# Kernel tuning notes

Hardware: AMD Instinct MI355X
Metric: run time of the kernel (lower is better)

## Reference

```python
import jax, jax.numpy as jnp
import numpy as np

N, M, H, K, C_IN, C_OUT, P_DIM = 25000, 25000, 32, 15, 128, 128, 3
KP_EXTENT = 1.2
RADIUS = 2.5


def setup_inputs() -> dict:
    key = jax.random.key(0)
    k1, k2, k3, k4, k5, k6 = jax.random.split(key, 6)
    x = jax.random.normal(k1, (M, C_IN), dtype=jnp.float32)
    q_pts = jax.random.uniform(k2, (N, P_DIM), dtype=jnp.float32) * (2.0 * RADIUS)
    s_pts = jax.random.uniform(k3, (M, P_DIM), dtype=jnp.float32) * (2.0 * RADIUS)
    # indices in [0, M]; index == M is the shadow neighbor
    neighb_inds = jax.random.randint(k4, (N, H), 0, M + 1, dtype=jnp.int64)
    # kernel points roughly inside the sphere of given radius
    kernel_points = jax.random.normal(k5, (K, P_DIM), dtype=jnp.float32) * (RADIUS * 0.5)
    # kaiming-like scale for weights [K, C_in, C_out]
    weights = jax.random.normal(k6, (K, C_IN, C_OUT), dtype=jnp.float32) * (1.0 / np.sqrt(C_IN))
    return {"x": x, "q_pts": q_pts, "s_pts": s_pts, "neighb_inds": neighb_inds,
            "kernel_points": kernel_points, "weights": weights}


def reference(x, q_pts, s_pts, neighb_inds, kernel_points, weights):
    # Add shadow point far away and zero shadow feature row
    s_pad = jnp.concatenate([s_pts, jnp.full((1, P_DIM), 1e6, dtype=s_pts.dtype)], axis=0)
    x_pad = jnp.concatenate([x, jnp.zeros((1, C_IN), dtype=x.dtype)], axis=0)

    # neighbors relative to each query point: [N, H, p_dim]
    neighbors = s_pad[neighb_inds] - q_pts[:, None, :]
    # differences to kernel points: [N, H, K, p_dim]
    differences = neighbors[:, :, None, :] - kernel_points[None, None, :, :]
    sq_distances = jnp.sum(differences * differences, axis=-1)  # [N, H, K]

    # linear influence, clipped at 0
    all_weights = jnp.clip(1.0 - jnp.sqrt(sq_distances) / KP_EXTENT, 0.0, None)
    all_weights = jnp.transpose(all_weights, (0, 2, 1))  # [N, K, H]

    neighb_x = x_pad[neighb_inds]                        # [N, H, C_in]
    weighted_features = jnp.matmul(all_weights, neighb_x)  # [N, K, C_in]

    # per-kernel-point matmul and sum over kernel points
    out = jnp.einsum('nkc,kcd->nd', weighted_features, weights)  # [N, C_out]
    return out
```

## Files before the change

### kernel.cpp

```cpp
#include <hip/hip_runtime.h>
#include <hip/hip_bf16.h>

#define N_Q   25000
#define M_S   25000
#define C_INV 128

typedef unsigned short ushortT;
typedef unsigned short us8 __attribute__((ext_vector_type(8)));
typedef unsigned short us4 __attribute__((ext_vector_type(4)));
typedef short s8v __attribute__((ext_vector_type(8)));
typedef float f32x4 __attribute__((ext_vector_type(4)));

#define GAS __attribute__((address_space(1)))
#define LAS __attribute__((address_space(3)))

__device__ __forceinline__ float b2f(ushortT u) {
    unsigned v = ((unsigned)u) << 16;
    return __builtin_bit_cast(float, v);
}
__device__ __forceinline__ ushortT f2b(float f) {
    __hip_bfloat16 h = __float2bfloat16(f);
    return __builtin_bit_cast(ushortT, h);
}

__global__ void k_convert_x(const float* __restrict__ x, ushortT* __restrict__ xb) {
    int i = blockIdx.x * 256 + threadIdx.x;
    const int n4 = (M_S * C_INV) / 4;
    if (i >= n4) return;
    float4 v = ((const float4*)x)[i];
    us4 o;
    o[0] = f2b(v.x); o[1] = f2b(v.y); o[2] = f2b(v.z); o[3] = f2b(v.w);
    ((us4*)xb)[i] = o;
}

__global__ void k_build_wfrag2(const float* __restrict__ W, ushortT* __restrict__ wf) {
    int o = blockIdx.x * 256 + threadIdx.x;
    if (o >= 262144) return;
    int j   = o & 7;
    int l   = (o >> 3) & 63;
    int db  = (o >> 9) & 7;
    int ks  = o >> 12;
    int p   = ks * 32 + ((l >> 4) * 8) + j;
    int ci  = p >> 8;
    int rem = p & 255;
    int ls  = rem >> 2;
    int r   = rem & 3;
    int k   = (ls >> 4) * 4 + r;
    int c   = ci * 16 + (ls & 15);
    int d   = db * 16 + (l & 15);
    wf[o] = (k < 15) ? f2b(W[((size_t)k * 128 + c) * 128 + d]) : (ushortT)0;
}

__global__ void k_build_wfrag(const float* __restrict__ W, ushortT* __restrict__ wf) {
    int o = blockIdx.x * 256 + threadIdx.x;
    if (o >= 1920 * 128) return;
    int j  = o & 7;
    int l  = (o >> 3) & 63;
    int db = (o >> 9) & 7;
    int ks = o >> 12;
    int r  = ks * 32 + ((l >> 4) * 8) + j;
    int d  = db * 16 + (l & 15);
    wf[o] = f2b(W[r * 128 + d]);
}

__global__ __launch_bounds__(512, 4) void k_ab(
    const float* __restrict__ qp, const float* __restrict__ sp,
    const int* __restrict__ nb, const float* __restrict__ kp,
    const ushortT* __restrict__ xbf, ushortT* __restrict__ wf_out)
{
    __shared__ __align__(16) ushortT s_w[16 * 512];
    __shared__ int s_idx[16 * 32];

    const int t   = threadIdx.x;
    const int l   = t & 63;
    const int w   = t >> 6;
    const int blk = blockIdx.x;

    {
        const int q  = t >> 5;
        const int h  = t & 31;
        const int qg = blk * 16 + q;
        const int qc = (qg < N_Q) ? qg : (N_Q - 1);
        const float qx = qp[qc * 3 + 0], qy = qp[qc * 3 + 1], qz = qp[qc * 3 + 2];
        int idx = (qg < N_Q) ? nb[qg * 32 + h] : M_S;
        const bool valid = ((unsigned)idx < (unsigned)M_S);
        const int idc = valid ? idx : 0;
        s_idx[q * 32 + h] = idc;
        float px, py, pz;
        if (valid) { px = sp[idc * 3]; py = sp[idc * 3 + 1]; pz = sp[idc * 3 + 2]; }
        else       { px = 1e6f; py = 1e6f; pz = 1e6f; }
        const float rx = px - qx, ry = py - qy, rz = pz - qz;
        #pragma unroll
        for (int k = 0; k < 15; ++k) {
            const float dx = rx - kp[k * 3 + 0];
            const float dy = ry - kp[k * 3 + 1];
            const float dz = rz - kp[k * 3 + 2];
            const float d2 = dx * dx + dy * dy + dz * dz;
            float wv = 1.0f - sqrtf(d2) * (1.0f / 1.2f);
            wv = (wv > 0.0f) ? wv : 0.0f;
            s_w[q * 512 + (h >> 3) * 128 + k * 8 + (h & 7)] = f2b(wv);
        }
        s_w[q * 512 + (h >> 3) * 128 + 15 * 8 + (h & 7)] = 0;
    }
    __syncthreads();

    const int c0 = l & 15;
    const int hg = l >> 4;

    s8v af[2];
    int ridx[2][8];
    #pragma unroll
    for (int qi = 0; qi < 2; ++qi) {
        const int q = w * 2 + qi;
        af[qi] = *(const s8v*)(s_w + q * 512 + hg * 128 + c0 * 8);
        #pragma unroll
        for (int j = 0; j < 8; ++j)
            ridx[qi][j] = s_idx[q * 32 + hg * 8 + j];
    }

    us4* wfo = (us4*)wf_out;

    #pragma unroll
    for (int qi = 0; qi < 2; ++qi) {
        const int qrow = blk * 16 + w * 2 + qi;
        const ushortT* rp[8];
        #pragma unroll
        for (int j = 0; j < 8; ++j)
            rp[j] = xbf + (size_t)ridx[qi][j] * 128 + c0;

        us8 xr[8];
        #pragma unroll
        for (int j = 0; j < 8; ++j) {
            #pragma unroll
            for (int ci = 0; ci < 8; ++ci)
                xr[ci][j] = rp[j][ci * 16];
        }
        #pragma unroll
        for (int ci = 0; ci < 8; ++ci) {
            f32x4 d = __builtin_amdgcn_mfma_f32_16x16x32_bf16(
                af[qi], __builtin_bit_cast(s8v, xr[ci]), (f32x4){0.f, 0.f, 0.f, 0.f}, 0, 0, 0);
            us4 o;
            o[0] = f2b(d[0]); o[1] = f2b(d[1]); o[2] = f2b(d[2]); o[3] = f2b(d[3]);
            wfo[(size_t)qrow * 512 + ci * 64 + l] = o;
        }
    }
}

__global__ __launch_bounds__(512, 4) void k_gemm(
    const ushortT* __restrict__ wf, const ushortT* __restrict__ wfrag,
    float* __restrict__ out)
{
    __shared__ __align__(16) ushortT sA[2][8192];

    const int t   = threadIdx.x;
    const int l   = t & 63;
    const int w   = t >> 6;
    const int blk = blockIdx.x;
    const int qg  = w >> 2;
    const int n0  = (w & 3) * 2;

    auto stage = [&](int c4, int buf) {
        #pragma unroll
        for (int u = 0; u < 2; ++u) {
            const int s    = u * 512 + t;
            const int q    = s >> 4;
            const int part = s & 15;
            const ushortT* src = wf + (size_t)(blk * 64 + q) * 2048 + c4 * 128
                               + ((part ^ (q & 7)) * 8);
            __builtin_amdgcn_global_load_lds((const GAS unsigned int*)(const void*)src,
                                             (LAS unsigned int*)(void*)(&sA[buf][(size_t)s * 8]),
                                             16, 0, 0);
        }
    };

    f32x4 a00 = {0.f,0.f,0.f,0.f}, a01 = {0.f,0.f,0.f,0.f};
    f32x4 a10 = {0.f,0.f,0.f,0.f}, a11 = {0.f,0.f,0.f,0.f};

    stage(0, 0);
    __syncthreads();

    for (int c4 = 0; c4 < 16; ++c4) {
        if (c4 < 15) stage(c4 + 1, (c4 + 1) & 1);
        const ushortT* A = sA[c4 & 1];
        const int q0 = qg * 32 + (l & 15);
        const int q1 = q0 + 16;
        #pragma unroll
        for (int kk = 0; kk < 4; ++kk) {
            const int ks = c4 * 4 + kk;
            const s8v b0 = *(const s8v*)(wfrag + ((size_t)(ks * 8 + n0    ) * 64 + l) * 8);
            const s8v b1 = *(const s8v*)(wfrag + ((size_t)(ks * 8 + n0 + 1) * 64 + l) * 8);
            const int eo = kk * 32 + (l >> 4) * 8;
            const s8v av0 = *(const s8v*)(A + q0 * 128 + (eo ^ ((q0 & 7) * 8)));
            const s8v av1 = *(const s8v*)(A + q1 * 128 + (eo ^ ((q1 & 7) * 8)));
            a00 = __builtin_amdgcn_mfma_f32_16x16x32_bf16(av0, b0, a00, 0, 0, 0);
            a01 = __builtin_amdgcn_mfma_f32_16x16x32_bf16(av0, b1, a01, 0, 0, 0);
            a10 = __builtin_amdgcn_mfma_f32_16x16x32_bf16(av1, b0, a10, 0, 0, 0);
            a11 = __builtin_amdgcn_mfma_f32_16x16x32_bf16(av1, b1, a11, 0, 0, 0);
        }
        __syncthreads();
    }

    #pragma unroll
    for (int r = 0; r < 4; ++r) {
        const int qa = blk * 64 + qg * 32 + (l >> 4) * 4 + r;
        const int qb = qa + 16;
        const int d0 = n0 * 16 + (l & 15);
        if (qa < N_Q) {
            out[(size_t)qa * 128 + d0]      = a00[r];
            out[(size_t)qa * 128 + d0 + 16] = a01[r];
        }
        if (qb < N_Q) {
            out[(size_t)qb * 128 + d0]      = a10[r];
            out[(size_t)qb * 128 + d0 + 16] = a11[r];
        }
    }
}

__global__ __launch_bounds__(256, 2) void k_main_fb(
    const float* __restrict__ qp, const float* __restrict__ sp,
    const int* __restrict__ nb, const float* __restrict__ kp,
    const ushortT* __restrict__ xbf, const ushortT* __restrict__ wfrag,
    float* __restrict__ out)
{
    __shared__ ushortT s_w[16][32][16];
    __shared__ int s_idx[16][32];
    __shared__ __align__(16) ushortT s_wf[16][1928];

    const int t   = threadIdx.x;
    const int blk = blockIdx.x;

    {
        const int q  = t >> 4;
        const int h0 = t & 15;
        const int qg = blk * 16 + q;
        const int qc = (qg < N_Q) ? qg : 0;
        const float qx = qp[qc * 3 + 0], qy = qp[qc * 3 + 1], qz = qp[qc * 3 + 2];
        #pragma unroll
        for (int i = 0; i < 2; ++i) {
            const int h  = h0 + 16 * i;
            int idx = (qg < N_Q) ? nb[qg * 32 + h] : M_S;
            const bool valid = ((unsigned)idx < (unsigned)M_S);
            s_idx[q][h] = valid ? idx : 0;
            float px, py, pz;
            if (valid) { px = sp[idx * 3]; py = sp[idx * 3 + 1]; pz = sp[idx * 3 + 2]; }
            else       { px = 1e6f; py = 1e6f; pz = 1e6f; }
            const float rx = px - qx, ry = py - qy, rz = pz - qz;
            #pragma unroll
            for (int k = 0; k < 15; ++k) {
                const float dx = rx - kp[k * 3 + 0];
                const float dy = ry - kp[k * 3 + 1];
                const float dz = rz - kp[k * 3 + 2];
                const float d2 = dx * dx + dy * dy + dz * dz;
                float wv = 1.0f - sqrtf(d2) * (1.0f / 1.2f);
                wv = (wv > 0.0f) ? wv : 0.0f;
                s_w[q][h][k] = f2b(wv);
            }
            s_w[q][h][15] = 0;
        }
    }
    __syncthreads();

    {
        const int q  = t >> 4;
        const int c0 = (t & 15) * 8;
        float acc[15][8];
        #pragma unroll
        for (int k = 0; k < 15; ++k)
            #pragma unroll
            for (int j = 0; j < 8; ++j) acc[k][j] = 0.0f;

        int idx0 = s_idx[q][0];
        us8 xv = *(const us8*)(xbf + (size_t)idx0 * C_INV + c0);
        for (int h = 0; h < 32; ++h) {
            const us8 xc = xv;
            if (h < 31) {
                int idn = s_idx[q][h + 1];
                xv = *(const us8*)(xbf + (size_t)idn * C_INV + c0);
            }
            const us8 w0 = *(const us8*)&s_w[q][h][0];
            const us8 w1 = *(const us8*)&s_w[q][h][8];
            float xf[8];
            #pragma unroll
            for (int j = 0; j < 8; ++j) xf[j] = b2f(xc[j]);
            #pragma unroll
            for (int k = 0; k < 15; ++k) {
                const float wk = b2f((k < 8) ? w0[k] : w1[k - 8]);
                #pragma unroll
                for (int j = 0; j < 8; ++j) acc[k][j] += wk * xf[j];
            }
        }
        #pragma unroll
        for (int k = 0; k < 15; ++k) {
            us8 o;
            #pragma unroll
            for (int j = 0; j < 8; ++j) o[j] = f2b(acc[k][j]);
            *(us8*)&s_wf[q][k * C_INV + c0] = o;
        }
    }
    __syncthreads();

    {
        const int lane = t & 63;
        const int wv   = t >> 6;
        const int db0  = wv * 2;
        const int arow = lane & 15;
        const int kofs = (lane >> 4) * 8;
        f32x4 acc0 = {0.f, 0.f, 0.f, 0.f};
        f32x4 acc1 = {0.f, 0.f, 0.f, 0.f};
        #pragma unroll 4
        for (int ks = 0; ks < 60; ++ks) {
            s8v a  = *(const s8v*)&s_wf[arow][ks * 32 + kofs];
            s8v b0 = *(const s8v*)(wfrag + ((size_t)(ks * 8 + db0) * 64 + lane) * 8);
            s8v b1 = *(const s8v*)(wfrag + ((size_t)(ks * 8 + db0 + 1) * 64 + lane) * 8);
            acc0 = __builtin_amdgcn_mfma_f32_16x16x32_bf16(a, b0, acc0, 0, 0, 0);
            acc1 = __builtin_amdgcn_mfma_f32_16x16x32_bf16(a, b1, acc1, 0, 0, 0);
        }
        #pragma unroll
        for (int r = 0; r < 4; ++r) {
            const int q  = (lane >> 4) * 4 + r;
            const int qg = blk * 16 + q;
            if (qg < N_Q) {
                out[(size_t)qg * 128 + db0 * 16 + (lane & 15)]       = acc0[r];
                out[(size_t)qg * 128 + (db0 + 1) * 16 + (lane & 15)] = acc1[r];
            }
        }
    }
}

extern "C" void kernel_launch(void* const* d_in, const int* in_sizes, int n_in,
                              void* d_out, int out_size, void* d_ws, size_t ws_size,
                              hipStream_t stream) {
    const float* x  = (const float*)d_in[0];
    const float* qp = (const float*)d_in[1];
    const float* sp = (const float*)d_in[2];
    const int*   nb = (const int*)d_in[3];
    const float* kp = (const float*)d_in[4];
    const float* W  = (const float*)d_in[5];
    float* out = (float*)d_out;

    const size_t xbf_b   = (size_t)M_S * C_INV * 2;
    const size_t wfrag_b = (size_t)2048 * 128 * 2;
    const size_t wf_b    = (size_t)25024 * 2048 * 2;

    ushortT* xbf   = (ushortT*)d_ws;
    ushortT* wfrag = (ushortT*)((char*)d_ws + xbf_b);
    ushortT* wfbuf = (ushortT*)((char*)d_ws + xbf_b + wfrag_b);

    k_convert_x<<<3125, 256, 0, stream>>>(x, xbf);

    if (ws_size >= xbf_b + wfrag_b + wf_b) {
        k_build_wfrag2<<<1024, 256, 0, stream>>>(W, wfrag);
        k_ab<<<(N_Q + 15) / 16, 512, 0, stream>>>(qp, sp, nb, kp, xbf, wfbuf);
        k_gemm<<<(N_Q + 63) / 64, 512, 0, stream>>>(wfbuf, wfrag, out);
    } else {
        k_build_wfrag<<<960, 256, 0, stream>>>(W, wfrag);
        k_main_fb<<<(N_Q + 15) / 16, 256, 0, stream>>>(qp, sp, nb, kp, xbf, wfrag, out);
    }
}
```

Before: 81.14 us.

## Gather neighbor features via LDS transpose reads and split-K gemm with atomics

The gather stage now uses 256-thread blocks of 8 queries. Neighbor feature rows are loaded with coalesced global_load_lds into LDS and then read back with ds_read_b64_tr_b16 to form MFMA B operands, replacing the scattered per-element 2-byte global loads. The second gemm drops its LDS staging in favor of direct global loads and splits the K dimension four ways across blocks, accumulating into a pre-zeroed output with float atomics. This targets the uncoalesced gather and raises parallelism in the gemm, at the cost of an extra zeroing kernel, atomic traffic, and dropped bounds checks in the gather kernel.

```diff
diff --git a/kernel.cpp b/kernel.cpp
--- a/kernel.cpp
+++ b/kernel.cpp
@@ -21,6 +21,12 @@
 __device__ __forceinline__ ushortT f2b(float f) {
     __hip_bfloat16 h = __float2bfloat16(f);
     return __builtin_bit_cast(ushortT, h);
+}
+__device__ __forceinline__ s8v mk8(us4 a, us4 b) {
+    us8 r;
+    r[0] = a[0]; r[1] = a[1]; r[2] = a[2]; r[3] = a[3];
+    r[4] = b[0]; r[5] = b[1]; r[6] = b[2]; r[7] = b[3];
+    return __builtin_bit_cast(s8v, r);
 }
 
 __global__ void k_convert_x(const float* __restrict__ x, ushortT* __restrict__ xb) {
@@ -63,13 +69,20 @@
     wf[o] = f2b(W[r * 128 + d]);
 }
 
-__global__ __launch_bounds__(512, 4) void k_ab(
+__global__ void k_zero(float* __restrict__ out) {
+    int i = blockIdx.x * 256 + threadIdx.x;
+    if (i < (N_Q * 128) / 4)
+        ((float4*)out)[i] = float4{0.f, 0.f, 0.f, 0.f};
+}
+
+__global__ __launch_bounds__(256, 6) void k_ab(
     const float* __restrict__ qp, const float* __restrict__ sp,
     const int* __restrict__ nb, const float* __restrict__ kp,
     const ushortT* __restrict__ xbf, ushortT* __restrict__ wf_out)
 {
-    __shared__ __align__(16) ushortT s_w[16 * 512];
-    __shared__ int s_idx[16 * 32];
+    __shared__ __align__(16) ushortT s_w[8 * 512];
+    __shared__ int s_idx[8 * 32];
+    __shared__ __align__(16) ushortT s_x[4][2048];
 
     const int t   = threadIdx.x;
     const int l   = t & 63;
@@ -79,10 +92,9 @@
     {
         const int q  = t >> 5;
         const int h  = t & 31;
-        const int qg = blk * 16 + q;
-        const int qc = (qg < N_Q) ? qg : (N_Q - 1);
-        const float qx = qp[qc * 3 + 0], qy = qp[qc * 3 + 1], qz = qp[qc * 3 + 2];
-        int idx = (qg < N_Q) ? nb[qg * 32 + h] : M_S;
+        const int qg = blk * 8 + q;
+        const float qx = qp[qg * 3 + 0], qy = qp[qg * 3 + 1], qz = qp[qg * 3 + 2];
+        int idx = nb[qg * 32 + h];
         const bool valid = ((unsigned)idx < (unsigned)M_S);
         const int idc = valid ? idx : 0;
         s_idx[q * 32 + h] = idc;
@@ -104,114 +116,115 @@
     }
     __syncthreads();
 
-    const int c0 = l & 15;
-    const int hg = l >> 4;
-
-    s8v af[2];
-    int ridx[2][8];
-    #pragma unroll
+    const int g = l >> 4;
+    const int c = l & 15;
+    us4* wfo = (us4*)wf_out;
+
+    LAS ushortT* trp = (LAS ushortT*)(void*)(&s_x[w][g * 128 + c * 4]);
+
     for (int qi = 0; qi < 2; ++qi) {
-        const int q = w * 2 + qi;
-        af[qi] = *(const s8v*)(s_w + q * 512 + hg * 128 + c0 * 8);
-        #pragma unroll
-        for (int j = 0; j < 8; ++j)
-            ridx[qi][j] = s_idx[q * 32 + hg * 8 + j];
-    }
-
-    us4* wfo = (us4*)wf_out;
-
-    #pragma unroll
-    for (int qi = 0; qi < 2; ++qi) {
-        const int qrow = blk * 16 + w * 2 + qi;
-        const ushortT* rp[8];
-        #pragma unroll
-        for (int j = 0; j < 8; ++j)
-            rp[j] = xbf + (size_t)ridx[qi][j] * 128 + c0;
-
-        us8 xr[8];
-        #pragma unroll
-        for (int j = 0; j < 8; ++j) {
-            #pragma unroll
-            for (int ci = 0; ci < 8; ++ci)
-                xr[ci][j] = rp[j][ci * 16];
-        }
-        #pragma unroll
-        for (int ci = 0; ci < 8; ++ci) {
-            f32x4 d = __builtin_amdgcn_mfma_f32_16x16x32_bf16(
-                af[qi], __builtin_bit_cast(s8v, xr[ci]), (f32x4){0.f, 0.f, 0.f, 0.f}, 0, 0, 0);
-            us4 o;
-            o[0] = f2b(d[0]); o[1] = f2b(d[1]); o[2] = f2b(d[2]); o[3] = f2b(d[3]);
-            wfo[(size_t)qrow * 512 + ci * 64 + l] = o;
-        }
-    }
-}
-
-__global__ __launch_bounds__(512, 4) void k_gemm(
+        const int q    = w * 2 + qi;
+        const int qrow = blk * 8 + q;
+        const s8v af   = *(const s8v*)(s_w + q * 512 + g * 128 + c * 8);
+        const int myid = s_idx[q * 32 + (l >> 1)];
+        const ushortT* srcb = xbf + (size_t)myid * 128 + (l & 1) * 8;
+
+        #pragma unroll
+        for (int hf = 0; hf < 2; ++hf) {
+            #pragma unroll
+            for (int ci = 0; ci < 4; ++ci) {
+                __builtin_amdgcn_global_load_lds(
+                    (const GAS unsigned int*)(const void*)(srcb + (hf * 4 + ci) * 16),
+                    (LAS unsigned int*)(void*)(&s_x[w][ci * 512]), 16, 0, 0);
+            }
+            asm volatile("s_waitcnt vmcnt(0)" ::: "memory");
+            __builtin_amdgcn_sched_barrier(0);
+
+            us4 ta0, tb0, ta1, tb1, ta2, tb2, ta3, tb3;
+            asm volatile(
+                "ds_read_b64_tr_b16 %0, %8 offset:0\n\t"
+                "ds_read_b64_tr_b16 %1, %8 offset:128\n\t"
+                "ds_read_b64_tr_b16 %2, %8 offset:1024\n\t"
+                "ds_read_b64_tr_b16 %3, %8 offset:1152\n\t"
+                "ds_read_b64_tr_b16 %4, %8 offset:2048\n\t"
+                "ds_read_b64_tr_b16 %5, %8 offset:2176\n\t"
+                "ds_read_b64_tr_b16 %6, %8 offset:3072\n\t"
+                "ds_read_b64_tr_b16 %7, %8 offset:3200\n\t"
+                "s_waitcnt lgkmcnt(0)"
+                : "=&v"(ta0), "=&v"(tb0), "=&v"(ta1), "=&v"(tb1),
+                  "=&v"(ta2), "=&v"(tb2), "=&v"(ta3), "=&v"(tb3)
+                : "v"(trp));
+            __builtin_amdgcn_sched_barrier(0);
+
+            const s8v b0 = mk8(ta0, tb0);
+            const s8v b1 = mk8(ta1, tb1);
+            const s8v b2 = mk8(ta2, tb2);
+            const s8v b3 = mk8(ta3, tb3);
+
+            #pragma unroll
+            for (int ci = 0; ci < 4; ++ci) {
+                const s8v bf = (ci == 0) ? b0 : (ci == 1) ? b1 : (ci == 2) ? b2 : b3;
+                f32x4 d = __builtin_amdgcn_mfma_f32_16x16x32_bf16(
+                    af, bf, (f32x4){0.f, 0.f, 0.f, 0.f}, 0, 0, 0);
+                us4 o;
+                o[0] = f2b(d[0]); o[1] = f2b(d[1]); o[2] = f2b(d[2]); o[3] = f2b(d[3]);
+                wfo[(size_t)qrow * 512 + (hf * 4 + ci) * 64 + l] = o;
+            }
+        }
+    }
+}
+
+__global__ __launch_bounds__(256, 6) void k_gemm(
     const ushortT* __restrict__ wf, const ushortT* __restrict__ wfrag,
     float* __restrict__ out)
 {
-    __shared__ __align__(16) ushortT sA[2][8192];
-
-    const int t   = threadIdx.x;
-    const int l   = t & 63;
-    const int w   = t >> 6;
-    const int blk = blockIdx.x;
-    const int qg  = w >> 2;
-    const int n0  = (w & 3) * 2;
-
-    auto stage = [&](int c4, int buf) {
-        #pragma unroll
-        for (int u = 0; u < 2; ++u) {
-            const int s    = u * 512 + t;
-            const int q    = s >> 4;
-            const int part = s & 15;
-            const ushortT* src = wf + (size_t)(blk * 64 + q) * 2048 + c4 * 128
-                               + ((part ^ (q & 7)) * 8);
-            __builtin_amdgcn_global_load_lds((const GAS unsigned int*)(const void*)src,
-                                             (LAS unsigned int*)(void*)(&sA[buf][(size_t)s * 8]),
-                                             16, 0, 0);
-        }
-    };
-
-    f32x4 a00 = {0.f,0.f,0.f,0.f}, a01 = {0.f,0.f,0.f,0.f};
-    f32x4 a10 = {0.f,0.f,0.f,0.f}, a11 = {0.f,0.f,0.f,0.f};
-
-    stage(0, 0);
-    __syncthreads();
-
-    for (int c4 = 0; c4 < 16; ++c4) {
-        if (c4 < 15) stage(c4 + 1, (c4 + 1) & 1);
-        const ushortT* A = sA[c4 & 1];
-        const int q0 = qg * 32 + (l & 15);
-        const int q1 = q0 + 16;
-        #pragma unroll
-        for (int kk = 0; kk < 4; ++kk) {
-            const int ks = c4 * 4 + kk;
-            const s8v b0 = *(const s8v*)(wfrag + ((size_t)(ks * 8 + n0    ) * 64 + l) * 8);
-            const s8v b1 = *(const s8v*)(wfrag + ((size_t)(ks * 8 + n0 + 1) * 64 + l) * 8);
-            const int eo = kk * 32 + (l >> 4) * 8;
-            const s8v av0 = *(const s8v*)(A + q0 * 128 + (eo ^ ((q0 & 7) * 8)));
-            const s8v av1 = *(const s8v*)(A + q1 * 128 + (eo ^ ((q1 & 7) * 8)));
-            a00 = __builtin_amdgcn_mfma_f32_16x16x32_bf16(av0, b0, a00, 0, 0, 0);
-            a01 = __builtin_amdgcn_mfma_f32_16x16x32_bf16(av0, b1, a01, 0, 0, 0);
-            a10 = __builtin_amdgcn_mfma_f32_16x16x32_bf16(av1, b0, a10, 0, 0, 0);
-            a11 = __builtin_amdgcn_mfma_f32_16x16x32_bf16(av1, b1, a11, 0, 0, 0);
-        }
-        __syncthreads();
+    const int t    = threadIdx.x;
+    const int l    = t & 63;
+    const int w    = t >> 6;
+    const int blk  = blockIdx.x;
+    const int tile = blk >> 2;
+    const int ksl  = blk & 3;
+    const int n0   = w * 2;
+    const int c    = l & 15;
+    const int g    = l >> 4;
+
+    f32x4 a00 = {0,0,0,0}, a01 = {0,0,0,0};
+    f32x4 a10 = {0,0,0,0}, a11 = {0,0,0,0};
+    f32x4 a20 = {0,0,0,0}, a21 = {0,0,0,0};
+    f32x4 a30 = {0,0,0,0}, a31 = {0,0,0,0};
+
+    const ushortT* ap = wf + ((size_t)(tile * 64 + c)) * 2048 + g * 8;
+
+    const int ks0 = ksl * 16;
+    #pragma unroll 4
+    for (int ks = ks0; ks < ks0 + 16; ++ks) {
+        const s8v b0 = *(const s8v*)(wfrag + ((size_t)(ks * 8 + n0    ) * 64 + l) * 8);
+        const s8v b1 = *(const s8v*)(wfrag + ((size_t)(ks * 8 + n0 + 1) * 64 + l) * 8);
+        const s8v va0 = *(const s8v*)(ap + (size_t)0 * 32768 + ks * 32);
+        const s8v va1 = *(const s8v*)(ap + (size_t)1 * 32768 + ks * 32);
+        const s8v va2 = *(const s8v*)(ap + (size_t)2 * 32768 + ks * 32);
+        const s8v va3 = *(const s8v*)(ap + (size_t)3 * 32768 + ks * 32);
+        a00 = __builtin_amdgcn_mfma_f32_16x16x32_bf16(va0, b0, a00, 0, 0, 0);
+        a01 = __builtin_amdgcn_mfma_f32_16x16x32_bf16(va0, b1, a01, 0, 0, 0);
+        a10 = __builtin_amdgcn_mfma_f32_16x16x32_bf16(va1, b0, a10, 0, 0, 0);
+        a11 = __builtin_amdgcn_mfma_f32_16x16x32_bf16(va1, b1, a11, 0, 0, 0);
+        a20 = __builtin_amdgcn_mfma_f32_16x16x32_bf16(va2, b0, a20, 0, 0, 0);
+        a21 = __builtin_amdgcn_mfma_f32_16x16x32_bf16(va2, b1, a21, 0, 0, 0);
+        a30 = __builtin_amdgcn_mfma_f32_16x16x32_bf16(va3, b0, a30, 0, 0, 0);
+        a31 = __builtin_amdgcn_mfma_f32_16x16x32_bf16(va3, b1, a31, 0, 0, 0);
     }
 
     #pragma unroll
-    for (int r = 0; r < 4; ++r) {
-        const int qa = blk * 64 + qg * 32 + (l >> 4) * 4 + r;
-        const int qb = qa + 16;
-        const int d0 = n0 * 16 + (l & 15);
-        if (qa < N_Q) {
-            out[(size_t)qa * 128 + d0]      = a00[r];
-            out[(size_t)qa * 128 + d0 + 16] = a01[r];
-        }
-        if (qb < N_Q) {
-            out[(size_t)qb * 128 + d0]      = a10[r];
-            out[(size_t)qb * 128 + d0 + 16] = a11[r];
+    for (int qq = 0; qq < 4; ++qq) {
+        const f32x4 v0 = (qq == 0) ? a00 : (qq == 1) ? a10 : (qq == 2) ? a20 : a30;
+        const f32x4 v1 = (qq == 0) ? a01 : (qq == 1) ? a11 : (qq == 2) ? a21 : a31;
+        #pragma unroll
+        for (int r = 0; r < 4; ++r) {
+            const int qrow = tile * 64 + qq * 16 + g * 4 + r;
+            if (qrow < N_Q) {
+                atomicAdd(&out[(size_t)qrow * 128 + n0 * 16 + c],        v0[r]);
+                atomicAdd(&out[(size_t)qrow * 128 + (n0 + 1) * 16 + c],  v1[r]);
+            }
         }
     }
 }
@@ -350,8 +363,9 @@
 
     if (ws_size >= xbf_b + wfrag_b + wf_b) {
         k_build_wfrag2<<<1024, 256, 0, stream>>>(W, wfrag);
-        k_ab<<<(N_Q + 15) / 16, 512, 0, stream>>>(qp, sp, nb, kp, xbf, wfbuf);
-        k_gemm<<<(N_Q + 63) / 64, 512, 0, stream>>>(wfbuf, wfrag, out);
+        k_zero<<<3125, 256, 0, stream>>>(out);
+        k_ab<<<3125, 256, 0, stream>>>(qp, sp, nb, kp, xbf, wfbuf);
+        k_gemm<<<391 * 4, 256, 0, stream>>>(wfbuf, wfrag, out);
     } else {
         k_build_wfrag<<<960, 256, 0, stream>>>(W, wfrag);
         k_main_fb<<<(N_Q + 15) / 16, 256, 0, stream>>>(qp, sp, nb, kp, xbf, wfrag, out);
```

Result: slower. 153.2 us (+88.8%).

## Split GEMM reduction dimension across two blocks and add partial-sum reduce kernel

Applied to the files above, without the earlier changes.

Replaces the single GEMM kernel with a split-K version that launches two blocks per 64-row tile, each covering half of the 2048-long reduction, writing partials to the output and a new workspace buffer. A separate reduce kernel then adds the two partials. This doubles the block count (391 to 782) to better fill the 256 CUs, at the cost of an extra 12.8MB write/read round trip and an additional kernel launch. It requires a larger workspace; otherwise the old path is used.

```diff
diff --git a/kernel.cpp b/kernel.cpp
--- a/kernel.cpp
+++ b/kernel.cpp
@@ -146,7 +146,90 @@
     }
 }
 
-__global__ __launch_bounds__(512, 4) void k_gemm(
+__global__ __launch_bounds__(512, 4) void k_gemm_split(
+    const ushortT* __restrict__ wf, const ushortT* __restrict__ wfrag,
+    float* __restrict__ out, float* __restrict__ p1)
+{
+    __shared__ __align__(16) ushortT sA[2][8192];
+
+    const int t    = threadIdx.x;
+    const int l    = t & 63;
+    const int w    = t >> 6;
+    const int blk  = blockIdx.x;
+    const int tile = blk >> 1;
+    const int ksl  = blk & 1;
+    const int qg   = w >> 2;
+    const int n0   = (w & 3) * 2;
+
+    auto stage = [&](int c4, int buf) {
+        #pragma unroll
+        for (int u = 0; u < 2; ++u) {
+            const int s    = u * 512 + t;
+            const int q    = s >> 4;
+            const int part = s & 15;
+            const ushortT* src = wf + (size_t)(tile * 64 + q) * 2048 + c4 * 128
+                               + ((part ^ (q & 7)) * 8);
+            __builtin_amdgcn_global_load_lds((const GAS unsigned int*)(const void*)src,
+                                             (LAS unsigned int*)(void*)(&sA[buf][(size_t)s * 8]),
+                                             16, 0, 0);
+        }
+    };
+
+    f32x4 a00 = {0.f,0.f,0.f,0.f}, a01 = {0.f,0.f,0.f,0.f};
+    f32x4 a10 = {0.f,0.f,0.f,0.f}, a11 = {0.f,0.f,0.f,0.f};
+
+    const int c4beg = ksl * 8;
+    stage(c4beg, 0);
+    __syncthreads();
+
+    for (int c4 = c4beg; c4 < c4beg + 8; ++c4) {
+        if (c4 < c4beg + 7) stage(c4 + 1, (c4 + 1) & 1);
+        const ushortT* A = sA[c4 & 1];
+        const int q0 = qg * 32 + (l & 15);
+        const int q1 = q0 + 16;
+        #pragma unroll
+        for (int kk = 0; kk < 4; ++kk) {
+            const int ks = c4 * 4 + kk;
+            const s8v b0 = *(const s8v*)(wfrag + ((size_t)(ks * 8 + n0    ) * 64 + l) * 8);
+            const s8v b1 = *(const s8v*)(wfrag + ((size_t)(ks * 8 + n0 + 1) * 64 + l) * 8);
+            const int eo = kk * 32 + (l >> 4) * 8;
+            const s8v av0 = *(const s8v*)(A + q0 * 128 + (eo ^ ((q0 & 7) * 8)));
+            const s8v av1 = *(const s8v*)(A + q1 * 128 + (eo ^ ((q1 & 7) * 8)));
+            a00 = __builtin_amdgcn_mfma_f32_16x16x32_bf16(av0, b0, a00, 0, 0, 0);
+            a01 = __builtin_amdgcn_mfma_f32_16x16x32_bf16(av0, b1, a01, 0, 0, 0);
+            a10 = __builtin_amdgcn_mfma_f32_16x16x32_bf16(av1, b0, a10, 0, 0, 0);
+            a11 = __builtin_amdgcn_mfma_f32_16x16x32_bf16(av1, b1, a11, 0, 0, 0);
+        }
+        __syncthreads();
+    }
+
+    float* dst = ksl ? p1 : out;
+    #pragma unroll
+    for (int r = 0; r < 4; ++r) {
+        const int qa = tile * 64 + qg * 32 + (l >> 4) * 4 + r;
+        const int qb = qa + 16;
+        const int d0 = n0 * 16 + (l & 15);
+        if (qa < N_Q) {
+            dst[(size_t)qa * 128 + d0]      = a00[r];
+            dst[(size_t)qa * 128 + d0 + 16] = a01[r];
+        }
+        if (qb < N_Q) {
+            dst[(size_t)qb * 128 + d0]      = a10[r];
+            dst[(size_t)qb * 128 + d0 + 16] = a11[r];
+        }
+    }
+}
+
+__global__ void k_reduce(float* __restrict__ out, const float* __restrict__ p1) {
+    int i = blockIdx.x * 256 + threadIdx.x;
+    if (i >= (N_Q * 128) / 4) return;
+    float4 a = ((const float4*)out)[i];
+    float4 b = ((const float4*)p1)[i];
+    a.x += b.x; a.y += b.y; a.z += b.z; a.w += b.w;
+    ((float4*)out)[i] = a;
+}
+
+__global__ __launch_bounds__(512, 4) void k_gemm_full(
     const ushortT* __restrict__ wf, const ushortT* __restrict__ wfrag,
     float* __restrict__ out)
 {
@@ -341,17 +424,24 @@
     const size_t xbf_b   = (size_t)M_S * C_INV * 2;
     const size_t wfrag_b = (size_t)2048 * 128 * 2;
     const size_t wf_b    = (size_t)25024 * 2048 * 2;
+    const size_t p1_b    = (size_t)25024 * 128 * 4;
 
     ushortT* xbf   = (ushortT*)d_ws;
     ushortT* wfrag = (ushortT*)((char*)d_ws + xbf_b);
     ushortT* wfbuf = (ushortT*)((char*)d_ws + xbf_b + wfrag_b);
+    float*   p1    = (float*)((char*)d_ws + xbf_b + wfrag_b + wf_b);
 
     k_convert_x<<<3125, 256, 0, stream>>>(x, xbf);
 
-    if (ws_size >= xbf_b + wfrag_b + wf_b) {
+    if (ws_size >= xbf_b + wfrag_b + wf_b + p1_b) {
         k_build_wfrag2<<<1024, 256, 0, stream>>>(W, wfrag);
         k_ab<<<(N_Q + 15) / 16, 512, 0, stream>>>(qp, sp, nb, kp, xbf, wfbuf);
-        k_gemm<<<(N_Q + 63) / 64, 512, 0, stream>>>(wfbuf, wfrag, out);
+        k_gemm_split<<<391 * 2, 512, 0, stream>>>(wfbuf, wfrag, out, p1);
+        k_reduce<<<3125, 256, 0, stream>>>(out, p1);
+    } else if (ws_size >= xbf_b + wfrag_b + wf_b) {
+        k_build_wfrag2<<<1024, 256, 0, stream>>>(W, wfrag);
+        k_ab<<<(N_Q + 15) / 16, 512, 0, stream>>>(qp, sp, nb, kp, xbf, wfbuf);
+        k_gemm_full<<<(N_Q + 63) / 64, 512, 0, stream>>>(wfbuf, wfrag, out);
     } else {
         k_build_wfrag<<<960, 256, 0, stream>>>(W, wfrag);
         k_main_fb<<<(N_Q + 15) / 16, 256, 0, stream>>>(qp, sp, nb, kp, xbf, wfrag, out);
```

After: 90.36 us. 1.11x slower.
